# Kernel optimization log

Measured on AMD Instinct MI355X. Metric: run time of the kernel, lower is better.

Reference implementation:

```python
import jax, jax.numpy as jnp
import numpy as np

NUM_LATENT, NUM_TRASH, DEPTH = 7, 3, 4
N_QUBITS = NUM_LATENT + NUM_TRASH            # 10, embedding/entangler wires
N_WIRES = NUM_LATENT + 2 * NUM_TRASH + 1     # 14, total device wires (wire 0 = MSB, PennyLane convention)
AUX = N_WIRES - 1                            # swap-test ancilla (last wire)
BATCH = 256

_H = (np.array([[1.0, 1.0], [1.0, -1.0]]) / np.sqrt(2.0)).astype(np.complex64)
_CNOT = np.array([[1, 0, 0, 0], [0, 1, 0, 0], [0, 0, 0, 1], [0, 0, 1, 0]], dtype=np.complex64)
_CSWAP = np.eye(8, dtype=np.complex64)
_CSWAP[[5, 6]] = _CSWAP[[6, 5]]              # swap targets iff control=1: |101> <-> |110>


def _rx(theta):
    # RX(theta) = [[cos(t/2), -i sin(t/2)], [-i sin(t/2), cos(t/2)]]; theta [...] -> [..., 2, 2]
    c = jnp.cos(theta / 2).astype(jnp.complex64)
    s = jnp.sin(theta / 2).astype(jnp.complex64) * (-1j)
    return jnp.stack([jnp.stack([c, s], -1), jnp.stack([s, c], -1)], -2)


def _apply_1q(state, gate, wire):
    # state [B, 2^W]; gate [2,2] (shared) or [B,2,2] (per-sample)
    B = state.shape[0]
    a, b = 2 ** wire, 2 ** (N_WIRES - wire - 1)
    s = state.reshape(B, a, 2, b)
    if gate.ndim == 3:
        s = jnp.einsum('bij,bajc->baic', gate, s)
    else:
        s = jnp.einsum('ij,bajc->baic', gate, s)
    return s.reshape(B, -1)


def _apply_kq(state, gate, wires):
    # general k-qubit constant gate on arbitrary (possibly non-adjacent) wires
    B = state.shape[0]
    k = len(wires)
    t = state.reshape((B,) + (2,) * N_WIRES)
    t = jnp.moveaxis(t, [w + 1 for w in wires], range(1, k + 1))
    t = t.reshape(B, 2 ** k, -1)
    t = jnp.einsum('ij,bjc->bic', jnp.asarray(gate), t)
    t = t.reshape((B,) + (2,) * N_WIRES)
    t = jnp.moveaxis(t, range(1, k + 1), [w + 1 for w in wires])
    return t.reshape(B, -1)


def _forward(features, weights):
    B = features.shape[0]
    state = jnp.zeros((B, 2 ** N_WIRES), jnp.complex64).at[:, 0].set(1.0)
    # AngleEmbedding(rotation='X'): per-sample RX(features[:, w]) on wire w
    g_emb = _rx(features)  # [B, n_qubits, 2, 2]
    for w in range(N_QUBITS):
        state = _apply_1q(state, g_emb[:, w], w)
    # BasicEntanglerLayers: per layer, RX(weights[l, w]) on each wire, then ring of CNOTs
    wts = weights.reshape(DEPTH, N_QUBITS)
    for l in range(DEPTH):
        g_l = _rx(wts[l])  # [n_qubits, 2, 2]
        for w in range(N_QUBITS):
            state = _apply_1q(state, g_l[w], w)
        for w in range(N_QUBITS):
            state = _apply_kq(state, _CNOT, [w, (w + 1) % N_QUBITS])
    # Swap test: H(aux); CSWAP(aux, latent+i, latent+trash+i); H(aux)
    state = _apply_1q(state, jnp.asarray(_H), AUX)
    for i in range(NUM_TRASH):
        state = _apply_kq(state, _CSWAP, [AUX, NUM_LATENT + i, NUM_LATENT + NUM_TRASH + i])
    state = _apply_1q(state, jnp.asarray(_H), AUX)
    # probs on aux wire (last wire -> innermost axis); return P(aux=1)
    p = jnp.sum(jnp.abs(state.reshape(B, 2 ** (N_WIRES - 1), 2)) ** 2, axis=1)
    return p[:, 1]


def setup_inputs() -> dict:
    key = jax.random.key(0)
    kf, kw = jax.random.split(key)
    features = jax.random.normal(kf, (BATCH, N_QUBITS), jnp.float32)
    weights = 0.01 * jax.random.uniform(kw, (DEPTH, N_QUBITS), jnp.float32)
    return {"features": features, "weights": weights}


def reference(features, weights):
    return _forward(features, weights)
```

## Files before the change

### kernel.cpp

```cpp
#include <hip/hip_runtime.h>
#include <math.h>


#define NQ     10
#define DIM    1024
#define NDEPTH 4
#define NGATE  (NQ + NDEPTH * NQ)

__device__ inline int cnot_ring_inv(int i) {
#pragma unroll
    for (int w = NQ - 1; w >= 0; --w) {
        int cb   = (i >> (NQ - 1 - w)) & 1;
        int tpos = NQ - 1 - ((w + 1) % NQ);
        i ^= cb << tpos;
    }
    return i;
}

__global__ __launch_bounds__(512) void qae_kernel(
    const float* __restrict__ features,
    const float* __restrict__ weights,
    float* __restrict__ out)
{
    __shared__ float sre[DIM];
    __shared__ float sim_[DIM];
    __shared__ float gc[NGATE];
    __shared__ float gs[NGATE];
    __shared__ float part[2];

    const int b   = blockIdx.x;
    const int tid = threadIdx.x;

    sre[tid]        = 0.0f;  sim_[tid]        = 0.0f;
    sre[tid + 512]  = 0.0f;  sim_[tid + 512]  = 0.0f;
    if (tid == 0) sre[0] = 1.0f;
    if (tid < NGATE) {
        float ang = (tid < NQ) ? features[b * NQ + tid] : weights[tid - NQ];
        float h = 0.5f * ang;
        gc[tid] = cosf(h);
        gs[tid] = sinf(h);
    }
    __syncthreads();

    auto rx = [&](int w, float c, float s) {
        int bitpos = NQ - 1 - w;
        int mask   = 1 << bitpos;
        int i0 = ((tid >> bitpos) << (bitpos + 1)) | (tid & (mask - 1));
        int i1 = i0 | mask;
        float a0r = sre[i0], a0i = sim_[i0];
        float a1r = sre[i1], a1i = sim_[i1];
        sre[i0]  = fmaf(c, a0r,  s * a1i);
        sim_[i0] = fmaf(c, a0i, -s * a1r);
        sre[i1]  = fmaf(c, a1r,  s * a0i);
        sim_[i1] = fmaf(c, a1i, -s * a0r);
    };

    for (int w = 0; w < NQ; ++w) {
        rx(w, gc[w], gs[w]);
        __syncthreads();
    }

    for (int l = 0; l < NDEPTH; ++l) {
        for (int w = 0; w < NQ; ++w) {
            int g = NQ + l * NQ + w;
            rx(w, gc[g], gs[g]);
            __syncthreads();
        }
        int j0 = tid, j1 = tid + 512;
        int s0 = cnot_ring_inv(j0);
        int s1 = cnot_ring_inv(j1);
        float r0 = sre[s0], m0 = sim_[s0];
        float r1 = sre[s1], m1 = sim_[s1];
        __syncthreads();
        sre[j0] = r0; sim_[j0] = m0;
        sre[j1] = r1; sim_[j1] = m1;
        __syncthreads();
    }

    float acc = 0.0f;
    if (tid < 128) {
        int i = tid << 3;
        acc = sre[i] * sre[i] + sim_[i] * sim_[i];
#pragma unroll
        for (int off = 32; off > 0; off >>= 1)
            acc += __shfl_down(acc, off, 64);
    }
    if (tid == 0)  part[0] = acc;
    if (tid == 64) part[1] = acc;
    __syncthreads();
    if (tid == 0)
        out[b] = 0.5f * (1.0f - (part[0] + part[1]));
}

extern "C" void kernel_launch(void* const* d_in, const int* in_sizes, int n_in,
                              void* d_out, int out_size, void* d_ws, size_t ws_size,
                              hipStream_t stream) {
    const float* features = (const float*)d_in[0];
    const float* weights  = (const float*)d_in[1];
    float*       out      = (float*)d_out;

    int B = in_sizes[0] / NQ;
    qae_kernel<<<B, 512, 0, stream>>>(features, weights, out);
}
```

Baseline: 63.95 us.

## Hold statevector in wave registers and fold CNOT permutations into gate masks

```diff
diff --git a/kernel.cpp b/kernel.cpp
--- a/kernel.cpp
+++ b/kernel.cpp
@@ -3,93 +3,128 @@
 
 
 #define NQ     10
-#define DIM    1024
-#define NDEPTH 4
-#define NGATE  (NQ + NDEPTH * NQ)
+#define DEPTHL 4
+#define NGATE  (NQ + DEPTHL * NQ)
 
-__device__ inline int cnot_ring_inv(int i) {
-#pragma unroll
+constexpr int lfwd_step(int i) {
+    for (int w = 0; w < NQ; ++w) {
+        int cb = (i >> (NQ - 1 - w)) & 1;
+        i ^= cb << (NQ - 1 - ((w + 1) % NQ));
+    }
+    return i;
+}
+constexpr int linv_step(int i) {
     for (int w = NQ - 1; w >= 0; --w) {
-        int cb   = (i >> (NQ - 1 - w)) & 1;
-        int tpos = NQ - 1 - ((w + 1) % NQ);
-        i ^= cb << tpos;
+        int cb = (i >> (NQ - 1 - w)) & 1;
+        i ^= cb << (NQ - 1 - ((w + 1) % NQ));
     }
     return i;
 }
 
-__global__ __launch_bounds__(512) void qae_kernel(
+static_assert(lfwd_step(linv_step(0x155)) == 0x155, "linv must invert lfwd");
+static_assert(linv_step(lfwd_step(0x2AB)) == 0x2AB, "lfwd must invert linv");
+
+struct MaskTab { int m[NGATE]; int row[3]; };
+
+constexpr MaskTab make_masks() {
+    MaskTab M{};
+    for (int w = 0; w < NQ; ++w) M.m[w] = 1 << (NQ - 1 - w);
+    for (int l = 0; l < DEPTHL; ++l)
+        for (int w = 0; w < NQ; ++w) {
+            int v = 1 << (NQ - 1 - w);
+            for (int k = 0; k < l; ++k) v = linv_step(v);
+            M.m[NQ + NQ * l + w] = v;
+        }
+    for (int p = 0; p < 3; ++p) {
+        int r = 0;
+        for (int j = 0; j < NQ; ++j) {
+            int y = 1 << j;
+            for (int k = 0; k < DEPTHL; ++k) y = lfwd_step(y);
+            r |= ((y >> p) & 1) << j;
+        }
+        M.row[p] = r;
+    }
+    return M;
+}
+
+constexpr MaskTab MK = make_masks();
+
+constexpr bool masks_ok() {
+    for (int g = 0; g < NGATE; ++g)
+        if (MK.m[g] <= 0 || MK.m[g] > 1023) return false;
+    return MK.row[0] && MK.row[1] && MK.row[2];
+}
+static_assert(masks_ok(), "gate masks must be nonzero 10-bit");
+
+__global__ __launch_bounds__(64) void qae_kernel(
     const float* __restrict__ features,
     const float* __restrict__ weights,
     float* __restrict__ out)
 {
-    __shared__ float sre[DIM];
-    __shared__ float sim_[DIM];
-    __shared__ float gc[NGATE];
-    __shared__ float gs[NGATE];
-    __shared__ float part[2];
+    const int b    = blockIdx.x;
+    const int lane = threadIdx.x;
 
-    const int b   = blockIdx.x;
-    const int tid = threadIdx.x;
-
-    sre[tid]        = 0.0f;  sim_[tid]        = 0.0f;
-    sre[tid + 512]  = 0.0f;  sim_[tid + 512]  = 0.0f;
-    if (tid == 0) sre[0] = 1.0f;
-    if (tid < NGATE) {
-        float ang = (tid < NQ) ? features[b * NQ + tid] : weights[tid - NQ];
+    float cg = 1.0f, sg = 0.0f;
+    if (lane < NGATE) {
+        float ang = (lane < NQ) ? features[b * NQ + lane] : weights[lane - NQ];
         float h = 0.5f * ang;
-        gc[tid] = cosf(h);
-        gs[tid] = sinf(h);
-    }
-    __syncthreads();
-
-    auto rx = [&](int w, float c, float s) {
-        int bitpos = NQ - 1 - w;
-        int mask   = 1 << bitpos;
-        int i0 = ((tid >> bitpos) << (bitpos + 1)) | (tid & (mask - 1));
-        int i1 = i0 | mask;
-        float a0r = sre[i0], a0i = sim_[i0];
-        float a1r = sre[i1], a1i = sim_[i1];
-        sre[i0]  = fmaf(c, a0r,  s * a1i);
-        sim_[i0] = fmaf(c, a0i, -s * a1r);
-        sre[i1]  = fmaf(c, a1r,  s * a0i);
-        sim_[i1] = fmaf(c, a1i, -s * a0r);
-    };
-
-    for (int w = 0; w < NQ; ++w) {
-        rx(w, gc[w], gs[w]);
-        __syncthreads();
+        cg = cosf(h);
+        sg = sinf(h);
     }
 
-    for (int l = 0; l < NDEPTH; ++l) {
-        for (int w = 0; w < NQ; ++w) {
-            int g = NQ + l * NQ + w;
-            rx(w, gc[g], gs[g]);
-            __syncthreads();
+    float tre[16], tim[16];
+#pragma unroll
+    for (int r = 0; r < 16; ++r) { tre[r] = 0.0f; tim[r] = 0.0f; }
+    if (lane == 0) tre[0] = 1.0f;
+
+#pragma unroll
+    for (int g = 0; g < NGATE; ++g) {
+        const int v  = MK.m[g];
+        const int lm = v >> 4;
+        const int rm = v & 15;
+        const float c = __shfl(cg, g, 64);
+        const float s = __shfl(sg, g, 64);
+
+        float pre[16], pim[16];
+        if (lm) {
+#pragma unroll
+            for (int r = 0; r < 16; ++r) {
+                pre[r] = __shfl_xor(tre[r ^ rm], lm, 64);
+                pim[r] = __shfl_xor(tim[r ^ rm], lm, 64);
+            }
+        } else {
+#pragma unroll
+            for (int r = 0; r < 16; ++r) {
+                pre[r] = tre[r ^ rm];
+                pim[r] = tim[r ^ rm];
+            }
         }
-        int j0 = tid, j1 = tid + 512;
-        int s0 = cnot_ring_inv(j0);
-        int s1 = cnot_ring_inv(j1);
-        float r0 = sre[s0], m0 = sim_[s0];
-        float r1 = sre[s1], m1 = sim_[s1];
-        __syncthreads();
-        sre[j0] = r0; sim_[j0] = m0;
-        sre[j1] = r1; sim_[j1] = m1;
-        __syncthreads();
+#pragma unroll
+        for (int r = 0; r < 16; ++r) {
+            tre[r] = fmaf(c, tre[r],  s * pim[r]);
+            tim[r] = fmaf(c, tim[r], -s * pre[r]);
+        }
     }
 
+    const int pl0 = __popc((MK.row[0] >> 4) & lane) & 1;
+    const int pl1 = __popc((MK.row[1] >> 4) & lane) & 1;
+    const int pl2 = __popc((MK.row[2] >> 4) & lane) & 1;
+
     float acc = 0.0f;
-    if (tid < 128) {
-        int i = tid << 3;
-        acc = sre[i] * sre[i] + sim_[i] * sim_[i];
 #pragma unroll
-        for (int off = 32; off > 0; off >>= 1)
-            acc += __shfl_down(acc, off, 64);
+    for (int r = 0; r < 16; ++r) {
+        const int pr0 = __popc(MK.row[0] & 15 & r) & 1;
+        const int pr1 = __popc(MK.row[1] & 15 & r) & 1;
+        const int pr2 = __popc(MK.row[2] & 15 & r) & 1;
+        const int bad = (pl0 ^ pr0) | (pl1 ^ pr1) | (pl2 ^ pr2);
+        if (!bad) acc += tre[r] * tre[r] + tim[r] * tim[r];
     }
-    if (tid == 0)  part[0] = acc;
-    if (tid == 64) part[1] = acc;
-    __syncthreads();
-    if (tid == 0)
-        out[b] = 0.5f * (1.0f - (part[0] + part[1]));
+
+#pragma unroll
+    for (int off = 32; off; off >>= 1)
+        acc += __shfl_xor(acc, off, 64);
+
+    if (lane == 0) out[b] = 0.5f * (1.0f - acc);
 }
 
 extern "C" void kernel_launch(void* const* d_in, const int* in_sizes, int n_in,
@@ -100,5 +135,5 @@
     float*       out      = (float*)d_out;
 
     int B = in_sizes[0] / NQ;
-    qae_kernel<<<B, 512, 0, stream>>>(features, weights, out);
+    qae_kernel<<<B, 64, 0, stream>>>(features, weights, out);
 }
```

New measurement: 64.67 us. About the same (+1.1%).
